# Optimization experiments

Measured on AMD Instinct MI355X. Metric: run time of the kernel, lower is better.

Reference implementation:

```python
import jax, jax.numpy as jnp
import numpy as np

N = 100000
E = 3200000
IN_C = 128
HID = 128


def setup_inputs() -> dict:
    key = jax.random.key(0)
    k1, k2, k3, k4, k5 = jax.random.split(key, 5)
    x = jax.random.normal(k1, (N, IN_C), dtype=jnp.float32)
    edge_index = jax.random.randint(k2, (2, E), 0, N, dtype=jnp.int64)
    edge_weight = jax.random.uniform(k3, (E,), dtype=jnp.float32)
    # GCNConv linear weight [out, in] (applied as x @ W.T), glorot-ish scale
    W = jax.random.normal(k4, (HID, IN_C), dtype=jnp.float32) / np.sqrt(IN_C)
    bias = jnp.zeros((HID,), dtype=jnp.float32)
    # PReLU per-channel alpha, torch default init 0.25
    alpha = jnp.full((HID,), 0.25, dtype=jnp.float32)
    return {"x": x, "edge_index": edge_index, "edge_weight": edge_weight,
            "W": W, "bias": bias, "alpha": alpha}


def reference(x, edge_index, edge_weight, W, bias, alpha):
    n = x.shape[0]
    # gcn_norm with self-loops (fill value 1.0)
    loop_idx = jnp.arange(n, dtype=edge_index.dtype)
    row = jnp.concatenate([edge_index[0], loop_idx])  # source
    col = jnp.concatenate([edge_index[1], loop_idx])  # target
    ew = jnp.concatenate([edge_weight, jnp.ones((n,), dtype=edge_weight.dtype)])
    deg = jax.ops.segment_sum(ew, col, num_segments=n)  # in-degree by weight
    dinv = jnp.where(deg > 0, jax.lax.rsqrt(deg), 0.0)
    norm = dinv[row] * ew * dinv[col]  # [E+N]
    # linear transform first (GCNConv order), then gather-scatter aggregation
    h = x @ W.T  # [N, HID]
    msgs = norm[:, None] * h[row]  # [E+N, HID]
    out = jax.ops.segment_sum(msgs, col, num_segments=n) + bias  # [N, HID]
    # PReLU with per-channel alpha
    return jnp.where(out > 0, out, alpha * out)
```

## Files before the change

### kernel.cpp

```cpp
#include <hip/hip_runtime.h>


#define NBLK    512
#define MAXBKT  1600
#define QSCALE  32767.0f

__device__ __forceinline__ unsigned bf16pack2(float a, float b) {
    unsigned ua = __float_as_uint(a);
    ua = (ua + 0x7fffu + ((ua >> 16) & 1u)) >> 16;
    unsigned ub = __float_as_uint(b);
    ub = (ub + 0x7fffu + ((ub >> 16) & 1u)) >> 16;
    return ua | (ub << 16);
}

__device__ __forceinline__ float2 bf16unpack2(unsigned u) {
    return make_float2(__uint_as_float(u << 16),
                       __uint_as_float(u & 0xffff0000u));
}

__global__ __launch_bounds__(256) void p1_hist(const int* __restrict__ col,
                                               unsigned* __restrict__ hist,
                                               int e, int nbkt, int epb) {
    __shared__ unsigned lh[MAXBKT];
    int b = blockIdx.x;
    for (int k = threadIdx.x; k < nbkt; k += 256) lh[k] = 0;
    __syncthreads();
    int s = b * epb, en = s + epb; if (en > e) en = e;
    for (int i = s + threadIdx.x; i < en; i += 256)
        atomicAdd(&lh[col[i] >> 6], 1u);
    __syncthreads();
    for (int k = threadIdx.x; k < nbkt; k += 256)
        hist[(size_t)k * NBLK + b] = lh[k];
}

__global__ __launch_bounds__(1024) void scan_partial2(
    const unsigned* __restrict__ a, unsigned* __restrict__ part, int m) {
    __shared__ unsigned red[1024];
    int t = threadIdx.x, i = blockIdx.x * 1024 + t;
    red[t] = (i < m) ? a[i] : 0;
    __syncthreads();
    #pragma unroll
    for (int d = 512; d > 0; d >>= 1) {
        if (t < d) red[t] += red[t + d];
        __syncthreads();
    }
    if (t == 0) part[blockIdx.x] = red[0];
}

__global__ __launch_bounds__(1024) void scan_base2(
    unsigned* __restrict__ part, int nb, int* __restrict__ offs, int n, int e) {
    __shared__ unsigned s[1024];
    int t = threadIdx.x;
    unsigned v = (t < nb) ? part[t] : 0;
    s[t] = v;
    __syncthreads();
    for (int d = 1; d < 1024; d <<= 1) {
        unsigned add = (t >= d) ? s[t - d] : 0;
        __syncthreads();
        s[t] += add;
        __syncthreads();
    }
    if (t < nb) part[t] = s[t] - v;
    if (t == 0) offs[n] = e;
}

__global__ __launch_bounds__(1024) void scan_write2(
    unsigned* __restrict__ a, const unsigned* __restrict__ part, int m) {
    __shared__ unsigned s[1024];
    int t = threadIdx.x, i = blockIdx.x * 1024 + t;
    unsigned v = (i < m) ? a[i] : 0;
    s[t] = v;
    __syncthreads();
    for (int d = 1; d < 1024; d <<= 1) {
        unsigned add = (t >= d) ? s[t - d] : 0;
        __syncthreads();
        s[t] += add;
        __syncthreads();
    }
    if (i < m) a[i] = part[blockIdx.x] + s[t] - v;
}

__global__ __launch_bounds__(256) void p2_scatter(
    const int* __restrict__ col, const int* __restrict__ row,
    const float* __restrict__ ew, const unsigned* __restrict__ base,
    unsigned long long* __restrict__ pay, int e, int nbkt, int epb) {
    __shared__ unsigned lbase[MAXBKT];
    __shared__ unsigned lcur[MAXBKT];
    int b = blockIdx.x;
    for (int k = threadIdx.x; k < nbkt; k += 256) {
        lbase[k] = base[(size_t)k * NBLK + b];
        lcur[k] = 0;
    }
    __syncthreads();
    int s = b * epb, en = s + epb; if (en > e) en = e;
    for (int i = s + threadIdx.x; i < en; i += 256) {
        int c = col[i];
        int bk = c >> 6;
        unsigned q  = (unsigned)(ew[i] * QSCALE + 0.5f);
        unsigned lo = ((unsigned)row[i] << 15) | q;
        unsigned rk = atomicAdd(&lcur[bk], 1u);
        pay[(size_t)lbase[bk] + rk] =
            ((unsigned long long)(unsigned)(c & 63) << 32) | lo;
    }
}

__global__ __launch_bounds__(256) void p3_build(
    const unsigned long long* __restrict__ pay,
    const unsigned* __restrict__ histBase,
    unsigned* __restrict__ csr, int* __restrict__ offs,
    float* __restrict__ dinv, int n, int nbkt, int e) {
    __shared__ unsigned cnt[64], wsum[64], lofs[64], cur[64];
    int bk = blockIdx.x;
    int zs = (int)histBase[(size_t)bk * NBLK];
    int ze = (bk + 1 < nbkt) ? (int)histBase[(size_t)(bk + 1) * NBLK] : e;
    int t = threadIdx.x;
    if (t < 64) { cnt[t] = 0; wsum[t] = 0; cur[t] = 0; }
    __syncthreads();
    for (int p = zs + t; p < ze; p += 256) {
        unsigned long long v = pay[p];
        int l = (int)(v >> 32) & 63;
        atomicAdd(&cnt[l], 1u);
        atomicAdd(&wsum[l], (unsigned)v & 0x7fffu);
    }
    __syncthreads();
    if (t == 0) {
        unsigned run = 0;
        for (int l = 0; l < 64; ++l) { lofs[l] = run; run += cnt[l]; }
    }
    __syncthreads();
    for (int p = zs + t; p < ze; p += 256) {
        unsigned long long v = pay[p];
        int l = (int)(v >> 32) & 63;
        unsigned rk = atomicAdd(&cur[l], 1u);
        csr[zs + lofs[l] + rk] = (unsigned)v;
    }
    if (t < 64) {
        int node = bk * 64 + t;
        if (node < n) {
            offs[node] = zs + (int)lofs[t];
            float dg = 1.0f + (float)wsum[t] * (1.0f / QSCALE);
            dinv[node] = rsqrtf(dg);
        }
    }
}

__global__ __launch_bounds__(256) void af_fill(const unsigned* __restrict__ csr,
                                               const float* __restrict__ dinv,
                                               float* __restrict__ af, int e) {
    int i = blockIdx.x * 256 + threadIdx.x;
    if (i < e) {
        unsigned v = csr[i];
        af[i] = dinv[v >> 15] * ((float)(v & 0x7fffu) * (1.0f / QSCALE));
    }
}

__global__ __launch_bounds__(256) void gemm_kernel(const float* __restrict__ x,
                                                   const float* __restrict__ W,
                                                   unsigned* __restrict__ h, int n) {
    __shared__ float Wt[128][128];
    int t = threadIdx.x;
    const float4* W4 = (const float4*)W;
    #pragma unroll
    for (int it = 0; it < 16; ++it) {
        int i = t + it * 256;
        float4 v = W4[i];
        int o  = i >> 5;
        int kb = (i & 31) << 2;
        Wt[kb + 0][o ^ (((kb + 0) & 7) << 2)] = v.x;
        Wt[kb + 1][o ^ (((kb + 1) & 7) << 2)] = v.y;
        Wt[kb + 2][o ^ (((kb + 2) & 7) << 2)] = v.z;
        Wt[kb + 3][o ^ (((kb + 3) & 7) << 2)] = v.w;
    }
    __syncthreads();

    int tc = t & 31;
    int rs = t >> 5;
    int r0 = blockIdx.x * 64 + rs * 8;
    if (r0 >= n) return;
    const float4* x4 = (const float4*)x;

    float acc[8][4];
    #pragma unroll
    for (int ri = 0; ri < 8; ++ri)
        #pragma unroll
        for (int j = 0; j < 4; ++j) acc[ri][j] = 0.0f;

    int rcnt = n - r0; if (rcnt > 8) rcnt = 8;

    if (rcnt == 8) {
        for (int kq = 0; kq < 32; ++kq) {
            int kb = kq << 2;
            float4 wv0 = *(const float4*)&Wt[kb + 0][(4 * tc) ^ (((kb + 0) & 7) << 2)];
            float4 wv1 = *(const float4*)&Wt[kb + 1][(4 * tc) ^ (((kb + 1) & 7) << 2)];
            float4 wv2 = *(const float4*)&Wt[kb + 2][(4 * tc) ^ (((kb + 2) & 7) << 2)];
            float4 wv3 = *(const float4*)&Wt[kb + 3][(4 * tc) ^ (((kb + 3) & 7) << 2)];
            #pragma unroll
            for (int ri = 0; ri < 8; ++ri) {
                float4 xv = x4[(size_t)(r0 + ri) * 32 + kq];
                acc[ri][0] += xv.x * wv0.x + xv.y * wv1.x + xv.z * wv2.x + xv.w * wv3.x;
                acc[ri][1] += xv.x * wv0.y + xv.y * wv1.y + xv.z * wv2.y + xv.w * wv3.y;
                acc[ri][2] += xv.x * wv0.z + xv.y * wv1.z + xv.z * wv2.z + xv.w * wv3.z;
                acc[ri][3] += xv.x * wv0.w + xv.y * wv1.w + xv.z * wv2.w + xv.w * wv3.w;
            }
        }
        uint2* h2 = (uint2*)h;
        #pragma unroll
        for (int ri = 0; ri < 8; ++ri)
            h2[(size_t)(r0 + ri) * 32 + tc] =
                make_uint2(bf16pack2(acc[ri][0], acc[ri][1]),
                           bf16pack2(acc[ri][2], acc[ri][3]));
    } else {
        for (int kq = 0; kq < 32; ++kq) {
            int kb = kq << 2;
            float4 wv0 = *(const float4*)&Wt[kb + 0][(4 * tc) ^ (((kb + 0) & 7) << 2)];
            float4 wv1 = *(const float4*)&Wt[kb + 1][(4 * tc) ^ (((kb + 1) & 7) << 2)];
            float4 wv2 = *(const float4*)&Wt[kb + 2][(4 * tc) ^ (((kb + 2) & 7) << 2)];
            float4 wv3 = *(const float4*)&Wt[kb + 3][(4 * tc) ^ (((kb + 3) & 7) << 2)];
            for (int ri = 0; ri < rcnt; ++ri) {
                float4 xv = x4[(size_t)(r0 + ri) * 32 + kq];
                acc[ri][0] += xv.x * wv0.x + xv.y * wv1.x + xv.z * wv2.x + xv.w * wv3.x;
                acc[ri][1] += xv.x * wv0.y + xv.y * wv1.y + xv.z * wv2.y + xv.w * wv3.y;
                acc[ri][2] += xv.x * wv0.z + xv.y * wv1.z + xv.z * wv2.z + xv.w * wv3.z;
                acc[ri][3] += xv.x * wv0.w + xv.y * wv1.w + xv.z * wv2.w + xv.w * wv3.w;
            }
        }
        uint2* h2 = (uint2*)h;
        for (int ri = 0; ri < rcnt; ++ri)
            h2[(size_t)(r0 + ri) * 32 + tc] =
                make_uint2(bf16pack2(acc[ri][0], acc[ri][1]),
                           bf16pack2(acc[ri][2], acc[ri][3]));
    }
}

__global__ __launch_bounds__(256) void aggregate_kernel(
    const unsigned* __restrict__ h, const unsigned* __restrict__ csr,
    const float* __restrict__ af, const int* __restrict__ offs,
    const float* __restrict__ dinv, const float* __restrict__ bias,
    const float* __restrict__ alpha, float* __restrict__ out, int n, int swzq) {
    int bid = blockIdx.x;
    int sb  = swzq ? ((bid & 7) * swzq + (bid >> 3)) : bid;
    int w = sb * 4 + (threadIdx.x >> 6);
    if (w >= n) return;
    int lane = threadIdx.x & 63;

    int beg = __builtin_amdgcn_readfirstlane(offs[w]);
    int end = __builtin_amdgcn_readfirstlane(offs[w + 1]);
    float ax = 0.0f, ay = 0.0f;

    int i = beg;
    int end4 = beg + ((end - beg) & ~3);
    for (; i < end4; i += 4) {
        unsigned s0 = csr[i]     >> 15, s1 = csr[i + 1] >> 15;
        unsigned s2 = csr[i + 2] >> 15, s3 = csr[i + 3] >> 15;
        float a0 = af[i],     a1 = af[i + 1];
        float a2 = af[i + 2], a3 = af[i + 3];
        unsigned u0 = h[(size_t)s0 * 64 + lane];
        unsigned u1 = h[(size_t)s1 * 64 + lane];
        unsigned u2 = h[(size_t)s2 * 64 + lane];
        unsigned u3 = h[(size_t)s3 * 64 + lane];
        float2 v0 = bf16unpack2(u0), v1 = bf16unpack2(u1);
        float2 v2 = bf16unpack2(u2), v3 = bf16unpack2(u3);
        ax += a0 * v0.x; ay += a0 * v0.y;
        ax += a1 * v1.x; ay += a1 * v1.y;
        ax += a2 * v2.x; ay += a2 * v2.y;
        ax += a3 * v3.x; ay += a3 * v3.y;
    }
    for (; i < end; ++i) {
        unsigned s = csr[i] >> 15;
        float a = af[i];
        float2 v = bf16unpack2(h[(size_t)s * 64 + lane]);
        ax += a * v.x; ay += a * v.y;
    }

    float dc = dinv[w];
    float2 hc = bf16unpack2(h[(size_t)w * 64 + lane]);
    ax += dc * hc.x; ay += dc * hc.y;

    float2 bv = ((const float2*)bias)[lane];
    float2 av = ((const float2*)alpha)[lane];
    float ox = ax * dc + bv.x;
    float oy = ay * dc + bv.y;
    ox = ox > 0.0f ? ox : av.x * ox;
    oy = oy > 0.0f ? oy : av.y * oy;
    ((float2*)out)[(size_t)w * 64 + lane] = make_float2(ox, oy);
}

extern "C" void kernel_launch(void* const* d_in, const int* in_sizes, int n_in,
                              void* d_out, int out_size, void* d_ws, size_t ws_size,
                              hipStream_t stream) {
    const float* x     = (const float*)d_in[0];
    const int*   ei    = (const int*)d_in[1];
    const float* ew    = (const float*)d_in[2];
    const float* W     = (const float*)d_in[3];
    const float* bias  = (const float*)d_in[4];
    const float* alpha = (const float*)d_in[5];
    float* out = (float*)d_out;

    const int n = in_sizes[0] / 128;
    const int e = in_sizes[1] / 2;
    const int* row = ei;
    const int* col = ei + e;

    const int nbkt = (n + 63) >> 6;
    const int m    = nbkt * NBLK;
    const int epb  = (e + NBLK - 1) / NBLK;
    const int nb2  = (m + 1023) / 1024;

    char* ws = (char*)d_ws;
    size_t off = 0;
    auto alloc = [&](size_t bytes) -> char* {
        char* p = ws + off;
        off = (off + bytes + 255) & ~(size_t)255;
        return p;
    };
    unsigned*           hist = (unsigned*)          alloc((size_t)m * 4);
    unsigned*           part = (unsigned*)          alloc((size_t)1024 * 4);
    int*                offs = (int*)               alloc((size_t)(n + 1) * 4);
    float*              dinv = (float*)             alloc((size_t)n * 4);
    unsigned long long* pay  = (unsigned long long*)alloc((size_t)e * 8);
    unsigned*           csr  = (unsigned*)          alloc((size_t)e * 4);
    float*              afv  = (float*)             alloc((size_t)e * 4);
    unsigned*           h    = (unsigned*)          alloc((size_t)n * 128 * 2);
    (void)ws_size; (void)n_in; (void)out_size;

    p1_hist<<<NBLK, 256, 0, stream>>>(col, hist, e, nbkt, epb);
    scan_partial2<<<nb2, 1024, 0, stream>>>(hist, part, m);
    scan_base2<<<1, 1024, 0, stream>>>(part, nb2, offs, n, e);
    scan_write2<<<nb2, 1024, 0, stream>>>(hist, part, m);
    p2_scatter<<<NBLK, 256, 0, stream>>>(col, row, ew, hist, pay, e, nbkt, epb);
    p3_build<<<nbkt, 256, 0, stream>>>(pay, hist, csr, offs, dinv, n, nbkt, e);
    af_fill<<<(e + 255) / 256, 256, 0, stream>>>(csr, dinv, afv, e);

    int gg = (n + 63) / 64;
    gemm_kernel<<<gg, 256, 0, stream>>>(x, W, h, n);

    int ga = (n + 3) / 4;
    int swzq = (ga % 8 == 0) ? ga / 8 : 0;
    aggregate_kernel<<<ga, 256, 0, stream>>>(h, csr, afv, offs, dinv,
                                             bias, alpha, out, n, swzq);
}
```

Before: 296.1 us.

## Pack quantized edge coefficient into CSR word and sort neighbors by source band

p3_build now sorts each destination's incoming edges into 16 coarse bands by source index, so gathers of h rows within a segment land in nearby memory and should get better cache locality. The per-edge normalized coefficient is requantized to 15 bits and packed into the CSR word. The aggregate kernel therefore reads one 4-byte stream per edge instead of two, using nontemporal loads for it and a nontemporal store for the output. The cost is extra quantization error on the edge coefficient and more shared-memory counters and atomics in the build kernel.

Result: no change. 294.4 us (-0.6%).

```diff
diff --git a/kernel.cpp b/kernel.cpp
--- a/kernel.cpp
+++ b/kernel.cpp
@@ -4,6 +4,9 @@
 #define NBLK    512
 #define MAXBKT  1600
 #define QSCALE  32767.0f
+#define SBS     16
+
+typedef float vfloat2 __attribute__((ext_vector_type(2)));
 
 __device__ __forceinline__ unsigned bf16pack2(float a, float b) {
     unsigned ua = __float_as_uint(a);
@@ -109,48 +112,71 @@
     const unsigned* __restrict__ histBase,
     unsigned* __restrict__ csr, int* __restrict__ offs,
     float* __restrict__ dinv, int n, int nbkt, int e) {
-    __shared__ unsigned cnt[64], wsum[64], lofs[64], cur[64];
+    __shared__ unsigned cnt[64][SBS], lofs[64][SBS], cur[64][SBS];
+    __shared__ unsigned wsum[64], tbase[64], ttot[64];
     int bk = blockIdx.x;
     int zs = (int)histBase[(size_t)bk * NBLK];
     int ze = (bk + 1 < nbkt) ? (int)histBase[(size_t)(bk + 1) * NBLK] : e;
     int t = threadIdx.x;
-    if (t < 64) { cnt[t] = 0; wsum[t] = 0; cur[t] = 0; }
+    for (int k = t; k < 64 * SBS; k += 256) {
+        (&cnt[0][0])[k] = 0;
+        (&cur[0][0])[k] = 0;
+    }
+    if (t < 64) wsum[t] = 0;
     __syncthreads();
     for (int p = zs + t; p < ze; p += 256) {
         unsigned long long v = pay[p];
         int l = (int)(v >> 32) & 63;
-        atomicAdd(&cnt[l], 1u);
-        atomicAdd(&wsum[l], (unsigned)v & 0x7fffu);
+        unsigned lo = (unsigned)v;
+        int sb = (int)((lo >> 15) >> 13);
+        atomicAdd(&cnt[l][sb], 1u);
+        atomicAdd(&wsum[l], lo & 0x7fffu);
+    }
+    __syncthreads();
+    if (t < 64) {
+        unsigned s = 0;
+        #pragma unroll
+        for (int j = 0; j < SBS; ++j) s += cnt[t][j];
+        ttot[t] = s;
     }
     __syncthreads();
     if (t == 0) {
         unsigned run = 0;
-        for (int l = 0; l < 64; ++l) { lofs[l] = run; run += cnt[l]; }
+        for (int l = 0; l < 64; ++l) { tbase[l] = run; run += ttot[l]; }
+    }
+    __syncthreads();
+    if (t < 64) {
+        unsigned run = tbase[t];
+        #pragma unroll
+        for (int j = 0; j < SBS; ++j) { lofs[t][j] = run; run += cnt[t][j]; }
     }
     __syncthreads();
     for (int p = zs + t; p < ze; p += 256) {
         unsigned long long v = pay[p];
         int l = (int)(v >> 32) & 63;
-        unsigned rk = atomicAdd(&cur[l], 1u);
-        csr[zs + lofs[l] + rk] = (unsigned)v;
+        unsigned lo = (unsigned)v;
+        int sb = (int)((lo >> 15) >> 13);
+        unsigned rk = atomicAdd(&cur[l][sb], 1u);
+        csr[zs + lofs[l][sb] + rk] = lo;
     }
     if (t < 64) {
         int node = bk * 64 + t;
         if (node < n) {
-            offs[node] = zs + (int)lofs[t];
+            offs[node] = zs + (int)tbase[t];
             float dg = 1.0f + (float)wsum[t] * (1.0f / QSCALE);
             dinv[node] = rsqrtf(dg);
         }
     }
 }
 
-__global__ __launch_bounds__(256) void af_fill(const unsigned* __restrict__ csr,
-                                               const float* __restrict__ dinv,
-                                               float* __restrict__ af, int e) {
+__global__ __launch_bounds__(256) void csr2_fill(const unsigned* __restrict__ csr,
+                                                 const float* __restrict__ dinv,
+                                                 unsigned* __restrict__ csr2, int e) {
     int i = blockIdx.x * 256 + threadIdx.x;
     if (i < e) {
         unsigned v = csr[i];
-        af[i] = dinv[v >> 15] * ((float)(v & 0x7fffu) * (1.0f / QSCALE));
+        float a = dinv[v >> 15] * ((float)(v & 0x7fffu) * (1.0f / QSCALE));
+        csr2[i] = (v & 0xffff8000u) | (unsigned)(a * QSCALE + 0.5f);
     }
 }
 
@@ -233,10 +259,10 @@
 }
 
 __global__ __launch_bounds__(256) void aggregate_kernel(
-    const unsigned* __restrict__ h, const unsigned* __restrict__ csr,
-    const float* __restrict__ af, const int* __restrict__ offs,
-    const float* __restrict__ dinv, const float* __restrict__ bias,
-    const float* __restrict__ alpha, float* __restrict__ out, int n, int swzq) {
+    const unsigned* __restrict__ h, const unsigned* __restrict__ csr2,
+    const int* __restrict__ offs, const float* __restrict__ dinv,
+    const float* __restrict__ bias, const float* __restrict__ alpha,
+    float* __restrict__ out, int n, int swzq) {
     int bid = blockIdx.x;
     int sb  = swzq ? ((bid & 7) * swzq + (bid >> 3)) : bid;
     int w = sb * 4 + (threadIdx.x >> 6);
@@ -250,26 +276,31 @@
     int i = beg;
     int end4 = beg + ((end - beg) & ~3);
     for (; i < end4; i += 4) {
-        unsigned s0 = csr[i]     >> 15, s1 = csr[i + 1] >> 15;
-        unsigned s2 = csr[i + 2] >> 15, s3 = csr[i + 3] >> 15;
-        float a0 = af[i],     a1 = af[i + 1];
-        float a2 = af[i + 2], a3 = af[i + 3];
-        unsigned u0 = h[(size_t)s0 * 64 + lane];
-        unsigned u1 = h[(size_t)s1 * 64 + lane];
-        unsigned u2 = h[(size_t)s2 * 64 + lane];
-        unsigned u3 = h[(size_t)s3 * 64 + lane];
-        float2 v0 = bf16unpack2(u0), v1 = bf16unpack2(u1);
-        float2 v2 = bf16unpack2(u2), v3 = bf16unpack2(u3);
-        ax += a0 * v0.x; ay += a0 * v0.y;
-        ax += a1 * v1.x; ay += a1 * v1.y;
-        ax += a2 * v2.x; ay += a2 * v2.y;
-        ax += a3 * v3.x; ay += a3 * v3.y;
+        unsigned v0 = __builtin_nontemporal_load(&csr2[i]);
+        unsigned v1 = __builtin_nontemporal_load(&csr2[i + 1]);
+        unsigned v2 = __builtin_nontemporal_load(&csr2[i + 2]);
+        unsigned v3 = __builtin_nontemporal_load(&csr2[i + 3]);
+        unsigned u0 = h[(size_t)(v0 >> 15) * 64 + lane];
+        unsigned u1 = h[(size_t)(v1 >> 15) * 64 + lane];
+        unsigned u2 = h[(size_t)(v2 >> 15) * 64 + lane];
+        unsigned u3 = h[(size_t)(v3 >> 15) * 64 + lane];
+        float a0 = (float)(v0 & 0x7fffu) * (1.0f / QSCALE);
+        float a1 = (float)(v1 & 0x7fffu) * (1.0f / QSCALE);
+        float a2 = (float)(v2 & 0x7fffu) * (1.0f / QSCALE);
+        float a3 = (float)(v3 & 0x7fffu) * (1.0f / QSCALE);
+        float2 h0 = bf16unpack2(u0), h1 = bf16unpack2(u1);
+        float2 h2 = bf16unpack2(u2), h3 = bf16unpack2(u3);
+        ax += a0 * h0.x; ay += a0 * h0.y;
+        ax += a1 * h1.x; ay += a1 * h1.y;
+        ax += a2 * h2.x; ay += a2 * h2.y;
+        ax += a3 * h3.x; ay += a3 * h3.y;
     }
     for (; i < end; ++i) {
-        unsigned s = csr[i] >> 15;
-        float a = af[i];
-        float2 v = bf16unpack2(h[(size_t)s * 64 + lane]);
-        ax += a * v.x; ay += a * v.y;
+        unsigned v = __builtin_nontemporal_load(&csr2[i]);
+        unsigned u = h[(size_t)(v >> 15) * 64 + lane];
+        float a = (float)(v & 0x7fffu) * (1.0f / QSCALE);
+        float2 hv = bf16unpack2(u);
+        ax += a * hv.x; ay += a * hv.y;
     }
 
     float dc = dinv[w];
@@ -282,7 +313,9 @@
     float oy = ay * dc + bv.y;
     ox = ox > 0.0f ? ox : av.x * ox;
     oy = oy > 0.0f ? oy : av.y * oy;
-    ((float2*)out)[(size_t)w * 64 + lane] = make_float2(ox, oy);
+    vfloat2 ov; ov.x = ox; ov.y = oy;
+    __builtin_nontemporal_store(ov,
+        (vfloat2*)&((float2*)out)[(size_t)w * 64 + lane]);
 }
 
 extern "C" void kernel_launch(void* const* d_in, const int* in_sizes, int n_in,
@@ -319,7 +352,7 @@
     float*              dinv = (float*)             alloc((size_t)n * 4);
     unsigned long long* pay  = (unsigned long long*)alloc((size_t)e * 8);
     unsigned*           csr  = (unsigned*)          alloc((size_t)e * 4);
-    float*              afv  = (float*)             alloc((size_t)e * 4);
+    unsigned*           csr2 = (unsigned*)          alloc((size_t)e * 4);
     unsigned*           h    = (unsigned*)          alloc((size_t)n * 128 * 2);
     (void)ws_size; (void)n_in; (void)out_size;
 
@@ -329,13 +362,13 @@
     scan_write2<<<nb2, 1024, 0, stream>>>(hist, part, m);
     p2_scatter<<<NBLK, 256, 0, stream>>>(col, row, ew, hist, pay, e, nbkt, epb);
     p3_build<<<nbkt, 256, 0, stream>>>(pay, hist, csr, offs, dinv, n, nbkt, e);
-    af_fill<<<(e + 255) / 256, 256, 0, stream>>>(csr, dinv, afv, e);
+    csr2_fill<<<(e + 255) / 256, 256, 0, stream>>>(csr, dinv, csr2, e);
 
     int gg = (n + 63) / 64;
     gemm_kernel<<<gg, 256, 0, stream>>>(x, W, h, n);
 
     int ga = (n + 3) / 4;
     int swzq = (ga % 8 == 0) ? ga / 8 : 0;
-    aggregate_kernel<<<ga, 256, 0, stream>>>(h, csr, afv, offs, dinv,
+    aggregate_kernel<<<ga, 256, 0, stream>>>(h, csr2, offs, dinv,
                                              bias, alpha, out, n, swzq);
 }
```
